# Performance work log

Hardware: AMD Instinct MI355X
Metric: run time of the kernel (lower is better)

## Reference

```python
import jax, jax.numpy as jnp
import numpy as np
import math

B, SQ, SK, D = 32, 2048, 2048, 128


def setup_inputs() -> dict:
    key = jax.random.key(0)
    kq, kk, kv = jax.random.split(key, 3)
    queries = jax.random.normal(kq, (B, SQ, D), dtype=jnp.float32)
    keys = jax.random.normal(kk, (B, SK, D), dtype=jnp.float32)
    values = jax.random.normal(kv, (B, SK, D), dtype=jnp.float32)
    # causal mask: True = masked (future positions), broadcast over batch
    causal = jnp.triu(jnp.ones((SQ, SK), dtype=bool), k=1)
    mask = jnp.broadcast_to(causal, (B, SQ, SK))
    return {"queries": queries, "keys": keys, "values": values, "mask": mask}


def reference(queries, keys, values, mask):
    d = queries.shape[-1]
    scale = 1.0 / math.sqrt(d)
    # [B, Sq, Sk] score matrix (the module materializes this explicitly)
    scores = jnp.einsum("bqd,bkd->bqk", queries, keys) * scale
    scores = jnp.where(mask, -jnp.inf, scores)
    attn = jax.nn.softmax(scores, axis=-1)
    # dropout p=0.0 -> identity (eval parity)
    return jnp.einsum("bqk,bkd->bqd", attn, values)
```

## Files before the change

kernel.cpp:

```cpp
#include <hip/hip_runtime.h>
#include <hip/hip_bf16.h>

#define NB   32
#define SQL  2048
#define SKL  2048
#define DH   128
#define QBLK 128
#define KBLK 64

#define KSTR 136
#define VSTR 72
#define PSTR 72

typedef __attribute__((ext_vector_type(4))) float f32x4;
typedef __attribute__((ext_vector_type(8))) short s16x8;

__device__ __forceinline__ unsigned int pk2(float lo, float hi) {
  unsigned short a = __builtin_bit_cast(unsigned short, __float2bfloat16(lo));
  unsigned short b = __builtin_bit_cast(unsigned short, __float2bfloat16(hi));
  return (unsigned int)a | ((unsigned int)b << 16);
}

__global__ __launch_bounds__(512, 2)
void attn_fwd(const float* __restrict__ Qg, const float* __restrict__ Kg,
              const float* __restrict__ Vg, float* __restrict__ Og) {
  __shared__ __align__(16) unsigned short smem[2*64*KSTR + 2*128*VSTR + 8*16*PSTR];

  const int tid  = threadIdx.x;
  const int wid  = tid >> 6;
  const int lane = tid & 63;
  const int g    = lane >> 4;
  const int ln   = lane & 15;

  const int i    = blockIdx.x;
  const int half = i >> 8;
  const int idx  = i & 255;
  const int b    = idx >> 3;
  const int q3   = idx & 7;
  const int qt   = half ? q3 : (15 - q3);
  const int qb   = qt * QBLK;
  const int nt   = 2*qt + 2;

  const float* Qb = Qg + (size_t)b * SQL * DH;
  const float* Kb = Kg + (size_t)b * SKL * DH;
  const float* Vb = Vg + (size_t)b * SKL * DH;
  float* Ob = Og + (size_t)b * SQL * DH;

  const float qscale = 0.08838834764831845f * 1.4426950408889634f;

  s16x8 qf[4];
  {
    const float* qr = Qb + (size_t)(qb + 16*wid + ln) * DH + 8*g;
    #pragma unroll
    for (int c = 0; c < 4; ++c) {
      f32x4 a  = *(const f32x4*)(qr + 32*c);
      f32x4 b4 = *(const f32x4*)(qr + 32*c + 4);
      s16x8 q8;
      #pragma unroll
      for (int j = 0; j < 4; ++j) {
        q8[j]     = (short)(unsigned short)(pk2(a[j]  * qscale, 0.f) & 0xFFFF);
        q8[j + 4] = (short)(unsigned short)(pk2(b4[j] * qscale, 0.f) & 0xFFFF);
      }
      qf[c] = q8;
    }
  }

  f32x4 oacc[8];
  #pragma unroll
  for (int ot = 0; ot < 8; ++ot) oacc[ot] = (f32x4){0.f, 0.f, 0.f, 0.f};
  float m_run = -1e30f;
  float l_run = 0.f;

  const int qglob = qb + 16*wid + ln;
  const int qmax  = qb + 16*wid + 15;

  const int kcol  = tid & 31;
  const int krow0 = tid >> 5;
  const int vkq   = tid & 15;
  const int vdq   = tid >> 4;

  f32x4 kpre[4], vpre[4];

  {
    const float* ks = Kb;
    #pragma unroll
    for (int it = 0; it < 4; ++it)
      kpre[it] = *(const f32x4*)(ks + (size_t)(krow0 + 16*it) * DH + 4*kcol);
    const float* vs = Vb + 4*vdq;
    #pragma unroll
    for (int j = 0; j < 4; ++j)
      vpre[j] = *(const f32x4*)(vs + (size_t)(4*vkq + j) * DH);
  }

  for (int t = 0; t < nt; ++t) {
    const int buf = t & 1;
    const int kb  = t * KBLK;

    {
      unsigned short* Kl = smem + buf * (64*KSTR);
      #pragma unroll
      for (int it = 0; it < 4; ++it) {
        f32x4 v = kpre[it];
        uint2 pk = make_uint2(pk2(v[0], v[1]), pk2(v[2], v[3]));
        *(uint2*)&Kl[(krow0 + 16*it)*KSTR + 4*kcol] = pk;
      }
      unsigned short* Vl = smem + 2*(64*KSTR) + buf * (128*VSTR);
      #pragma unroll
      for (int j2 = 0; j2 < 4; ++j2) {
        uint2 pk = make_uint2(pk2(vpre[0][j2], vpre[1][j2]),
                              pk2(vpre[2][j2], vpre[3][j2]));
        *(uint2*)&Vl[(4*vdq + j2)*VSTR + 4*vkq] = pk;
      }
    }

    if (t + 1 < nt) {
      const int kn = (t + 1) * KBLK;
      const float* ks = Kb + (size_t)kn * DH;
      #pragma unroll
      for (int it = 0; it < 4; ++it)
        kpre[it] = *(const f32x4*)(ks + (size_t)(krow0 + 16*it) * DH + 4*kcol);
      const float* vs = Vb + (size_t)kn * DH + 4*vdq;
      #pragma unroll
      for (int j = 0; j < 4; ++j)
        vpre[j] = *(const f32x4*)(vs + (size_t)(4*vkq + j) * DH);
    }

    asm volatile("s_waitcnt lgkmcnt(0)" ::: "memory");
    __builtin_amdgcn_s_barrier();
    __builtin_amdgcn_sched_barrier(0);

    if (kb <= qmax) {
      const unsigned short* Kl = smem + buf * (64*KSTR);
      const unsigned short* Vl = smem + 2*(64*KSTR) + buf * (128*VSTR);
      unsigned short* Pl = smem + 2*(64*KSTR) + 2*(128*VSTR) + wid*(16*PSTR);

      f32x4 sacc[4];
      #pragma unroll
      for (int m = 0; m < 4; ++m) sacc[m] = (f32x4){0.f, 0.f, 0.f, 0.f};
      __builtin_amdgcn_s_setprio(1);
      #pragma unroll
      for (int c = 0; c < 4; ++c) {
        #pragma unroll
        for (int m = 0; m < 4; ++m) {
          s16x8 kf = *(const s16x8*)&Kl[(16*m + ln)*KSTR + 8*g + 32*c];
          sacc[m] = __builtin_amdgcn_mfma_f32_16x16x32_bf16(kf, qf[c], sacc[m], 0, 0, 0);
        }
      }
      __builtin_amdgcn_s_setprio(0);

      if (kb + KBLK - 1 > qb + 16*wid) {
        #pragma unroll
        for (int m = 0; m < 4; ++m)
          #pragma unroll
          for (int r = 0; r < 4; ++r) {
            const int kk = kb + 16*m + 4*g + r;
            if (kk > qglob) sacc[m][r] = -1e30f;
          }
      }

      float tmax = sacc[0][0];
      #pragma unroll
      for (int m = 0; m < 4; ++m)
        #pragma unroll
        for (int r = 0; r < 4; ++r) tmax = fmaxf(tmax, sacc[m][r]);
      tmax = fmaxf(tmax, __shfl_xor(tmax, 16));
      tmax = fmaxf(tmax, __shfl_xor(tmax, 32));
      const float mnew  = fmaxf(m_run, tmax);
      const float alpha = exp2f(m_run - mnew);
      float lsum = 0.f;
      unsigned int pw[4][2];
      #pragma unroll
      for (int m = 0; m < 4; ++m) {
        float p0 = exp2f(sacc[m][0] - mnew);
        float p1 = exp2f(sacc[m][1] - mnew);
        float p2 = exp2f(sacc[m][2] - mnew);
        float p3 = exp2f(sacc[m][3] - mnew);
        lsum += (p0 + p1) + (p2 + p3);
        pw[m][0] = pk2(p0, p1);
        pw[m][1] = pk2(p2, p3);
      }
      lsum += __shfl_xor(lsum, 16);
      lsum += __shfl_xor(lsum, 32);
      l_run = l_run * alpha + lsum;
      m_run = mnew;

      float ar[4];
      #pragma unroll
      for (int r = 0; r < 4; ++r) ar[r] = __shfl(alpha, 4*g + r);
      #pragma unroll
      for (int ot = 0; ot < 8; ++ot)
        #pragma unroll
        for (int r = 0; r < 4; ++r) oacc[ot][r] *= ar[r];

      {
        unsigned short* prow = Pl + ln*PSTR;
        #pragma unroll
        for (int m = 0; m < 4; ++m) {
          *(unsigned int*)&prow[16*m + 4*g]     = pw[m][0];
          *(unsigned int*)&prow[16*m + 4*g + 2] = pw[m][1];
        }
      }

      s16x8 pf[2];
      #pragma unroll
      for (int c2 = 0; c2 < 2; ++c2)
        pf[c2] = *(const s16x8*)&Pl[ln*PSTR + 8*g + 32*c2];
      __builtin_amdgcn_s_setprio(1);
      #pragma unroll
      for (int ot = 0; ot < 8; ++ot) {
        #pragma unroll
        for (int c2 = 0; c2 < 2; ++c2) {
          s16x8 vf = *(const s16x8*)&Vl[(16*ot + ln)*VSTR + 8*g + 32*c2];
          oacc[ot] = __builtin_amdgcn_mfma_f32_16x16x32_bf16(pf[c2], vf, oacc[ot], 0, 0, 0);
        }
      }
      __builtin_amdgcn_s_setprio(0);
    }
  }

  const float linv = 1.0f / l_run;
  float lr[4];
  #pragma unroll
  for (int r = 0; r < 4; ++r) lr[r] = __shfl(linv, 4*g + r);
  float* orow = Ob + (size_t)(qb + 16*wid) * DH + ln;
  #pragma unroll
  for (int ot = 0; ot < 8; ++ot)
    #pragma unroll
    for (int r = 0; r < 4; ++r)
      orow[(size_t)(4*g + r) * DH + 16*ot] = oacc[ot][r] * lr[r];
}

extern "C" void kernel_launch(void* const* d_in, const int* in_sizes, int n_in,
                              void* d_out, int out_size, void* d_ws, size_t ws_size,
                              hipStream_t stream) {
  const float* Q = (const float*)d_in[0];
  const float* K = (const float*)d_in[1];
  const float* V = (const float*)d_in[2];
  float* O = (float*)d_out;
  dim3 grid(NB * (SQL / QBLK));
  dim3 block(512);
  attn_fwd<<<grid, block, 0, stream>>>(Q, K, V, O);
}
```

Measured before the change: 103.6 us.

## Pre-convert K/V to swizzled bf16 tiles and stream them via direct global-to-LDS loads

Adds a prep kernel that converts K and V from fp32 to bf16 once per call, storing them in a workspace as XOR-swizzled 16KB tiles, with V transposed. The attention kernel then stages tiles straight into LDS with global_load_lds, double-buffered two tiles ahead. This removes the repeated fp32 loads, per-block conversions and register staging of K/V, which were redone by every query block of a batch. The cost is an extra kernel launch and a workspace round-trip, plus a change to an XOR-swizzled LDS layout and a raised occupancy hint (launch_bounds 512,4 with 80KB shared memory).

```diff
diff --git a/kernel.cpp b/kernel.cpp
--- a/kernel.cpp
+++ b/kernel.cpp
@@ -3,17 +3,15 @@
 
 #define NB   32
 #define SQL  2048
-#define SKL  2048
 #define DH   128
 #define QBLK 128
 #define KBLK 64
-
-#define KSTR 136
-#define VSTR 72
-#define PSTR 72
+#define NKT  (SQL / KBLK)
+#define TILEB 16384
 
 typedef __attribute__((ext_vector_type(4))) float f32x4;
 typedef __attribute__((ext_vector_type(8))) short s16x8;
+typedef __attribute__((ext_vector_type(4))) unsigned int u32x4;
 
 __device__ __forceinline__ unsigned int pk2(float lo, float hi) {
   unsigned short a = __builtin_bit_cast(unsigned short, __float2bfloat16(lo));
@@ -21,10 +19,60 @@
   return (unsigned int)a | ((unsigned int)b << 16);
 }
 
-__global__ __launch_bounds__(512, 2)
-void attn_fwd(const float* __restrict__ Qg, const float* __restrict__ Kg,
-              const float* __restrict__ Vg, float* __restrict__ Og) {
-  __shared__ __align__(16) unsigned short smem[2*64*KSTR + 2*128*VSTR + 8*16*PSTR];
+#define AS1(p) ((const __attribute__((address_space(1))) void*)(p))
+#define AS3(p) ((__attribute__((address_space(3))) void*)(p))
+
+__global__ __launch_bounds__(256)
+void prep_kv(const float* __restrict__ Kg, const float* __restrict__ Vg,
+             char* __restrict__ wsK, char* __restrict__ wsV) {
+  const int blk = blockIdx.x;
+  const int b   = blk >> 5;
+  const int kt  = blk & 31;
+  const int tid = threadIdx.x;
+  const float* Ksrc = Kg + ((size_t)b * SQL + (size_t)kt * KBLK) * DH;
+  const float* Vsrc = Vg + ((size_t)b * SQL + (size_t)kt * KBLK) * DH;
+  char* Kdst = wsK + (size_t)blk * TILEB;
+  char* Vdst = wsV + (size_t)blk * TILEB;
+
+  {
+    const int q16 = tid & 15;
+    const int r0  = tid >> 4;
+    #pragma unroll
+    for (int it = 0; it < 4; ++it) {
+      const int r = r0 + 16 * it;
+      const float* src = Ksrc + (size_t)r * DH + 8 * q16;
+      f32x4 a = *(const f32x4*)(src);
+      f32x4 d = *(const f32x4*)(src + 4);
+      u32x4 w;
+      w[0] = pk2(a[0], a[1]); w[1] = pk2(a[2], a[3]);
+      w[2] = pk2(d[0], d[1]); w[3] = pk2(d[2], d[3]);
+      *(u32x4*)(Kdst + ((r * 256 + 16 * q16) ^ ((r & 7) << 4))) = w;
+    }
+  }
+  {
+    const int kq = tid & 15;
+    const int dq = tid >> 4;
+    #pragma unroll
+    for (int it = 0; it < 2; ++it) {
+      const int d0 = 4 * dq + 64 * it;
+      f32x4 rv[4];
+      #pragma unroll
+      for (int j = 0; j < 4; ++j)
+        rv[j] = *(const f32x4*)(Vsrc + (size_t)(4 * kq + j) * DH + d0);
+      #pragma unroll
+      for (int j2 = 0; j2 < 4; ++j2) {
+        const int dd = d0 + j2;
+        uint2 w = make_uint2(pk2(rv[0][j2], rv[1][j2]), pk2(rv[2][j2], rv[3][j2]));
+        *(uint2*)(Vdst + ((dd * 128 + 8 * kq) ^ ((dd & 7) << 4))) = w;
+      }
+    }
+  }
+}
+
+__global__ __launch_bounds__(512, 4)
+void attn_fwd(const float* __restrict__ Qg, const char* __restrict__ wsK,
+              const char* __restrict__ wsV, float* __restrict__ Og) {
+  __shared__ __align__(16) char smem[81920];
 
   const int tid  = threadIdx.x;
   const int wid  = tid >> 6;
@@ -39,101 +87,65 @@
   const int q3   = idx & 7;
   const int qt   = half ? q3 : (15 - q3);
   const int qb   = qt * QBLK;
-  const int nt   = 2*qt + 2;
+  const int nt   = 2 * qt + 2;
 
   const float* Qb = Qg + (size_t)b * SQL * DH;
-  const float* Kb = Kg + (size_t)b * SKL * DH;
-  const float* Vb = Vg + (size_t)b * SKL * DH;
   float* Ob = Og + (size_t)b * SQL * DH;
+  const char* Ktiles = wsK + (size_t)b * NKT * TILEB;
+  const char* Vtiles = wsV + (size_t)b * NKT * TILEB;
 
   const float qscale = 0.08838834764831845f * 1.4426950408889634f;
 
   s16x8 qf[4];
   {
-    const float* qr = Qb + (size_t)(qb + 16*wid + ln) * DH + 8*g;
+    const float* qr = Qb + (size_t)(qb + 16 * wid + ln) * DH + 8 * g;
     #pragma unroll
     for (int c = 0; c < 4; ++c) {
-      f32x4 a  = *(const f32x4*)(qr + 32*c);
-      f32x4 b4 = *(const f32x4*)(qr + 32*c + 4);
-      s16x8 q8;
-      #pragma unroll
-      for (int j = 0; j < 4; ++j) {
-        q8[j]     = (short)(unsigned short)(pk2(a[j]  * qscale, 0.f) & 0xFFFF);
-        q8[j + 4] = (short)(unsigned short)(pk2(b4[j] * qscale, 0.f) & 0xFFFF);
-      }
-      qf[c] = q8;
+      f32x4 a  = *(const f32x4*)(qr + 32 * c);
+      f32x4 b4 = *(const f32x4*)(qr + 32 * c + 4);
+      u32x4 w;
+      w[0] = pk2(a[0] * qscale, a[1] * qscale);
+      w[1] = pk2(a[2] * qscale, a[3] * qscale);
+      w[2] = pk2(b4[0] * qscale, b4[1] * qscale);
+      w[3] = pk2(b4[2] * qscale, b4[3] * qscale);
+      qf[c] = __builtin_bit_cast(s16x8, w);
     }
   }
 
   f32x4 oacc[8];
   #pragma unroll
   for (int ot = 0; ot < 8; ++ot) oacc[ot] = (f32x4){0.f, 0.f, 0.f, 0.f};
-  float m_run = -1e30f;
-  float l_run = 0.f;
-
-  const int qglob = qb + 16*wid + ln;
-  const int qmax  = qb + 16*wid + 15;
-
-  const int kcol  = tid & 31;
-  const int krow0 = tid >> 5;
-  const int vkq   = tid & 15;
-  const int vdq   = tid >> 4;
-
-  f32x4 kpre[4], vpre[4];
-
-  {
-    const float* ks = Kb;
-    #pragma unroll
-    for (int it = 0; it < 4; ++it)
-      kpre[it] = *(const f32x4*)(ks + (size_t)(krow0 + 16*it) * DH + 4*kcol);
-    const float* vs = Vb + 4*vdq;
-    #pragma unroll
-    for (int j = 0; j < 4; ++j)
-      vpre[j] = *(const f32x4*)(vs + (size_t)(4*vkq + j) * DH);
-  }
+  float m_run = -1e30f, l_run = 0.f;
+
+  const int qglob = qb + 16 * wid + ln;
+  const int qmax  = qb + 16 * wid + 15;
+
+  auto STAGE = [&](int t) {
+    const char* ks = Ktiles + (size_t)t * TILEB + wid * 2048 + lane * 16;
+    const char* vs = Vtiles + (size_t)t * TILEB + wid * 2048 + lane * 16;
+    char* kl = smem + (t & 1) * 16384 + wid * 2048;
+    char* vl = smem + 32768 + (t & 1) * 16384 + wid * 2048;
+    __builtin_amdgcn_global_load_lds(AS1(ks),        AS3(kl),        16, 0, 0);
+    __builtin_amdgcn_global_load_lds(AS1(ks + 1024), AS3(kl + 1024), 16, 0, 0);
+    __builtin_amdgcn_global_load_lds(AS1(vs),        AS3(vl),        16, 0, 0);
+    __builtin_amdgcn_global_load_lds(AS1(vs + 1024), AS3(vl + 1024), 16, 0, 0);
+  };
+
+  STAGE(0);
+  STAGE(1);
 
   for (int t = 0; t < nt; ++t) {
-    const int buf = t & 1;
-    const int kb  = t * KBLK;
-
-    {
-      unsigned short* Kl = smem + buf * (64*KSTR);
-      #pragma unroll
-      for (int it = 0; it < 4; ++it) {
-        f32x4 v = kpre[it];
-        uint2 pk = make_uint2(pk2(v[0], v[1]), pk2(v[2], v[3]));
-        *(uint2*)&Kl[(krow0 + 16*it)*KSTR + 4*kcol] = pk;
-      }
-      unsigned short* Vl = smem + 2*(64*KSTR) + buf * (128*VSTR);
-      #pragma unroll
-      for (int j2 = 0; j2 < 4; ++j2) {
-        uint2 pk = make_uint2(pk2(vpre[0][j2], vpre[1][j2]),
-                              pk2(vpre[2][j2], vpre[3][j2]));
-        *(uint2*)&Vl[(4*vdq + j2)*VSTR + 4*vkq] = pk;
-      }
-    }
-
-    if (t + 1 < nt) {
-      const int kn = (t + 1) * KBLK;
-      const float* ks = Kb + (size_t)kn * DH;
-      #pragma unroll
-      for (int it = 0; it < 4; ++it)
-        kpre[it] = *(const f32x4*)(ks + (size_t)(krow0 + 16*it) * DH + 4*kcol);
-      const float* vs = Vb + (size_t)kn * DH + 4*vdq;
-      #pragma unroll
-      for (int j = 0; j < 4; ++j)
-        vpre[j] = *(const f32x4*)(vs + (size_t)(4*vkq + j) * DH);
-    }
-
-    asm volatile("s_waitcnt lgkmcnt(0)" ::: "memory");
+    if (t == nt - 1) asm volatile("s_waitcnt vmcnt(0)" ::: "memory");
+    else             asm volatile("s_waitcnt vmcnt(4)" ::: "memory");
     __builtin_amdgcn_s_barrier();
     __builtin_amdgcn_sched_barrier(0);
 
+    const int kb = t * KBLK;
+    const char* Kl = smem + (t & 1) * 16384;
+    const char* Vl = smem + 32768 + (t & 1) * 16384;
+    char* Pw = smem + 65536 + wid * 2048;
+
     if (kb <= qmax) {
-      const unsigned short* Kl = smem + buf * (64*KSTR);
-      const unsigned short* Vl = smem + 2*(64*KSTR) + buf * (128*VSTR);
-      unsigned short* Pl = smem + 2*(64*KSTR) + 2*(128*VSTR) + wid*(16*PSTR);
-
       f32x4 sacc[4];
       #pragma unroll
       for (int m = 0; m < 4; ++m) sacc[m] = (f32x4){0.f, 0.f, 0.f, 0.f};
@@ -142,18 +154,18 @@
       for (int c = 0; c < 4; ++c) {
         #pragma unroll
         for (int m = 0; m < 4; ++m) {
-          s16x8 kf = *(const s16x8*)&Kl[(16*m + ln)*KSTR + 8*g + 32*c];
+          s16x8 kf = *(const s16x8*)(Kl + (((16 * m + ln) * 256 + 16 * g + 64 * c) ^ ((ln & 7) << 4)));
           sacc[m] = __builtin_amdgcn_mfma_f32_16x16x32_bf16(kf, qf[c], sacc[m], 0, 0, 0);
         }
       }
       __builtin_amdgcn_s_setprio(0);
 
-      if (kb + KBLK - 1 > qb + 16*wid) {
+      if (kb + KBLK - 1 > qb + 16 * wid) {
         #pragma unroll
         for (int m = 0; m < 4; ++m)
           #pragma unroll
           for (int r = 0; r < 4; ++r) {
-            const int kk = kb + 16*m + 4*g + r;
+            const int kk = kb + 16 * m + 4 * g + r;
             if (kk > qglob) sacc[m][r] = -1e30f;
           }
       }
@@ -186,48 +198,47 @@
 
       float ar[4];
       #pragma unroll
-      for (int r = 0; r < 4; ++r) ar[r] = __shfl(alpha, 4*g + r);
+      for (int r = 0; r < 4; ++r) ar[r] = __shfl(alpha, 4 * g + r);
       #pragma unroll
       for (int ot = 0; ot < 8; ++ot)
         #pragma unroll
         for (int r = 0; r < 4; ++r) oacc[ot][r] *= ar[r];
 
-      {
-        unsigned short* prow = Pl + ln*PSTR;
-        #pragma unroll
-        for (int m = 0; m < 4; ++m) {
-          *(unsigned int*)&prow[16*m + 4*g]     = pw[m][0];
-          *(unsigned int*)&prow[16*m + 4*g + 2] = pw[m][1];
-        }
-      }
+      #pragma unroll
+      for (int m = 0; m < 4; ++m)
+        *(uint2*)(Pw + ((ln * 128 + 32 * m + 8 * g) ^ ((ln & 7) << 4))) =
+            make_uint2(pw[m][0], pw[m][1]);
 
       s16x8 pf[2];
       #pragma unroll
       for (int c2 = 0; c2 < 2; ++c2)
-        pf[c2] = *(const s16x8*)&Pl[ln*PSTR + 8*g + 32*c2];
+        pf[c2] = *(const s16x8*)(Pw + ((ln * 128 + 16 * g + 64 * c2) ^ ((ln & 7) << 4)));
       __builtin_amdgcn_s_setprio(1);
       #pragma unroll
       for (int ot = 0; ot < 8; ++ot) {
         #pragma unroll
         for (int c2 = 0; c2 < 2; ++c2) {
-          s16x8 vf = *(const s16x8*)&Vl[(16*ot + ln)*VSTR + 8*g + 32*c2];
+          s16x8 vf = *(const s16x8*)(Vl + (((16 * ot + ln) * 128 + 16 * g + 64 * c2) ^ ((ln & 7) << 4)));
           oacc[ot] = __builtin_amdgcn_mfma_f32_16x16x32_bf16(pf[c2], vf, oacc[ot], 0, 0, 0);
         }
       }
       __builtin_amdgcn_s_setprio(0);
     }
+
+    __builtin_amdgcn_s_barrier();
+    if (t + 2 < nt) STAGE(t + 2);
   }
 
   const float linv = 1.0f / l_run;
   float lr[4];
   #pragma unroll
-  for (int r = 0; r < 4; ++r) lr[r] = __shfl(linv, 4*g + r);
-  float* orow = Ob + (size_t)(qb + 16*wid) * DH + ln;
+  for (int r = 0; r < 4; ++r) lr[r] = __shfl(linv, 4 * g + r);
+  float* orow = Ob + (size_t)(qb + 16 * wid) * DH + ln;
   #pragma unroll
   for (int ot = 0; ot < 8; ++ot)
     #pragma unroll
     for (int r = 0; r < 4; ++r)
-      orow[(size_t)(4*g + r) * DH + 16*ot] = oacc[ot][r] * lr[r];
+      orow[(size_t)(4 * g + r) * DH + 16 * ot] = oacc[ot][r] * lr[r];
 }
 
 extern "C" void kernel_launch(void* const* d_in, const int* in_sizes, int n_in,
@@ -237,7 +248,9 @@
   const float* K = (const float*)d_in[1];
   const float* V = (const float*)d_in[2];
   float* O = (float*)d_out;
-  dim3 grid(NB * (SQL / QBLK));
-  dim3 block(512);
-  attn_fwd<<<grid, block, 0, stream>>>(Q, K, V, O);
-}
+  char* wsK = (char*)d_ws;
+  char* wsV = (char*)d_ws + (size_t)NB * NKT * TILEB;
+
+  prep_kv<<<dim3(NB * NKT), dim3(256), 0, stream>>>(K, V, wsK, wsV);
+  attn_fwd<<<dim3(NB * (SQL / QBLK)), dim3(512), 0, stream>>>(Q, wsK, wsV, O);
+}
```

Result: faster. 100.4 us (-3.1%).
